# Optimization experiments

Measured on AMD Instinct MI355X. Metric: run time of the kernel, lower is better.

## Reference

```python
import jax, jax.numpy as jnp
import numpy as np

B, H, L, D = 16, 8, 512, 64
TEMPERATURE = 8.0  # sqrt(d_k)
MASK_SENTINEL = -10000.0
BIG_NEG = 1e9


def setup_inputs() -> dict:
    key = jax.random.key(0)
    kq, kk, kv, km = jax.random.split(key, 4)
    q = jax.random.normal(kq, (B * H, L, D), dtype=jnp.float32)
    k = jax.random.normal(kk, (B * H, L, D), dtype=jnp.float32)
    v = jax.random.normal(kv, (B * H, L, D), dtype=jnp.float32)
    mask = jnp.where(jax.random.bernoulli(km, 0.1, (B, L)), MASK_SENTINEL, 0.0).astype(jnp.float32)
    return {"q": q, "k": k, "v": v, "mask": mask, "n_head": H}


def reference(q, k, v, mask, n_head):
    # attn: [B*H, L, L]
    attn = jnp.einsum("bid,bjd->bij", q, k) / TEMPERATURE
    # masked_fill(mask == -10000, 1e9); other values subtracted as-is
    m = jnp.where(mask == MASK_SENTINEL, BIG_NEG, mask)          # [B, L]
    m_bh = jnp.repeat(m, n_head, axis=0)                          # [B*H, L], matches reshape(B*H, ...)
    # row mask (mask.unsqueeze(-1).repeat) and its transpose (column mask)
    attn = attn - m_bh[:, :, None] - m_bh[:, None, :]
    attn = jax.nn.softmax(attn, axis=2)
    # dropout in eval mode (identity) for the deterministic reference
    output = jnp.einsum("bij,bjd->bid", attn, v)
    return output, attn
```

## Files before the change

### kernel.cpp

```cpp
#include <hip/hip_runtime.h>
#include <stdint.h>

#define Ln 512
#define Dn 64
#define BHn 128
#define AOFF ((size_t)BHn*Ln*Dn)

typedef __attribute__((ext_vector_type(8))) short short8;
typedef __attribute__((ext_vector_type(4))) float f32x4;
typedef __attribute__((ext_vector_type(4))) unsigned int u32x4;
typedef __attribute__((ext_vector_type(2))) unsigned int u32x2;

__device__ __forceinline__ uint16_t f2bf(float f){
  uint32_t x = __float_as_uint(f);
  return (uint16_t)((x + 0x7FFFu + ((x>>16)&1u)) >> 16);
}
__device__ __forceinline__ float bf2f(uint16_t u){ return __uint_as_float(((uint32_t)u)<<16); }
__device__ __forceinline__ uint32_t pack2(float a, float b){
  return (uint32_t)f2bf(a) | ((uint32_t)f2bf(b)<<16);
}
__device__ __forceinline__ void gld16(const uint16_t* g, uint16_t* l){
  __builtin_amdgcn_global_load_lds(
      (const __attribute__((address_space(1))) void*)g,
      (__attribute__((address_space(3))) void*)l, 16, 0, 0);
}

extern "C" __global__ __launch_bounds__(256)
void attn_prep(const float* __restrict__ kg, const float* __restrict__ vg,
               uint16_t* __restrict__ khw, uint16_t* __restrict__ klw,
               uint16_t* __restrict__ vtw)
{
  const int t  = threadIdx.x;
  const int c  = blockIdx.x;
  const int bh = blockIdx.y;
  const size_t base = (size_t)bh*(Ln*Dn);
  const size_t wsb  = ((size_t)bh<<15) + ((size_t)c<<13);

  {
    const int sj  = t>>1, skh = t&1;
    const float* kr = kg + base + (size_t)(c*128 + sj)*Dn + skh*32;
    const int sx = (sj&7)<<3;
    #pragma unroll
    for (int w2=0; w2<4; ++w2){
      f32x4 x0 = *(const f32x4*)(kr + w2*8);
      f32x4 x1 = *(const f32x4*)(kr + w2*8 + 4);
      uint32_t hw[4], lw[4];
      #pragma unroll
      for (int pi=0; pi<4; ++pi){
        float a0 = (pi<2) ? x0[pi*2]   : x1[(pi-2)*2];
        float a1 = (pi<2) ? x0[pi*2+1] : x1[(pi-2)*2+1];
        uint16_t h0 = f2bf(a0), h1 = f2bf(a1);
        hw[pi] = (uint32_t)h0 | ((uint32_t)h1<<16);
        lw[pi] = (uint32_t)f2bf(a0 - bf2f(h0)) | ((uint32_t)f2bf(a1 - bf2f(h1))<<16);
      }
      const size_t di = wsb + sj*64 + ((skh*32 + w2*8) ^ sx);
      *(u32x4*)(khw + di) = (u32x4){hw[0],hw[1],hw[2],hw[3]};
      *(u32x4*)(klw + di) = (u32x4){lw[0],lw[1],lw[2],lw[3]};
    }
  }

  #pragma unroll
  for (int it=0; it<2; ++it){
    const int j0 = (t>>4)*4 + it*64;
    const int d0 = (t&15)*4;
    const float* vr = vg + base + (size_t)(c*128 + j0)*Dn + d0;
    f32x4 r0 = *(const f32x4*)(vr);
    f32x4 r1 = *(const f32x4*)(vr + Dn);
    f32x4 r2 = *(const f32x4*)(vr + 2*Dn);
    f32x4 r3 = *(const f32x4*)(vr + 3*Dn);
    #pragma unroll
    for (int qd=0; qd<4; ++qd){
      const int d = d0 + qd;
      u32x2 w; w.x = pack2(r0[qd], r1[qd]); w.y = pack2(r2[qd], r3[qd]);
      *(u32x2*)(vtw + wsb + d*128 + (j0 ^ ((d&7)<<3))) = w;
    }
  }
}

extern "C" __global__ __launch_bounds__(256, 2)
void attn_main2(const float* __restrict__ qg, const float* __restrict__ mg,
                const uint16_t* __restrict__ khw, const uint16_t* __restrict__ klw,
                const uint16_t* __restrict__ vtw, float* __restrict__ outg)
{
  __shared__ __align__(16) uint16_t BIG[32768];
  __shared__ float CMV[512];

  const int t    = threadIdx.x;
  const int lane = t & 63;
  const int wv   = t >> 6;
  const int li   = lane & 15;
  const int lq   = lane >> 4;
  const int kx   = (li&7)<<3;

  const int lin = blockIdx.x + (blockIdx.y << 3);
  const int xcd = lin & 7;
  const int jj  = lin >> 3;
  const int bh  = (xcd << 4) + (jj >> 3);
  const int b   = bh >> 3;
  const int i0  = (jj & 7)*64 + wv*16;

  const size_t base = (size_t)bh*(Ln*Dn);
  const float* mrow = mg + b*Ln;
  const size_t wsbh = (size_t)bh << 15;

  uint16_t* PW = BIG + 16384 + wv*2176;

  auto issueK = [&](int c, int bsel){
    const size_t so = wsbh + ((size_t)c<<13) + (wv<<11) + (lane<<3);
    uint16_t* dh = BIG + bsel*16384 + (wv<<11);
    #pragma unroll
    for (int i=0;i<4;++i){
      gld16(khw + so + i*512, dh + i*512);
      gld16(klw + so + i*512, dh + 8192 + i*512);
    }
  };
  auto issueV = [&](int c, int bsel){
    const size_t so = wsbh + ((size_t)c<<13) + (wv<<11) + (lane<<3);
    uint16_t* dv = BIG + bsel*8192 + (wv<<11);
    #pragma unroll
    for (int i=0;i<4;++i) gld16(vtw + so + i*512, dv + i*512);
  };

  const float* qrow = qg + base + (size_t)(i0 + li)*Dn;
  f32x4 qx0a = *(const f32x4*)(qrow + lq*8);
  f32x4 qx0b = *(const f32x4*)(qrow + lq*8 + 4);
  f32x4 qx1a = *(const f32x4*)(qrow + 32 + lq*8);
  f32x4 qx1b = *(const f32x4*)(qrow + 32 + lq*8 + 4);
  float m0 = mrow[t], m1 = mrow[t+256];
  float mv = mrow[i0 + li];

  issueK(0, 0);

  CMV[t]     = (m0 < -9000.f) ? 1e9f : m0;
  CMV[t+256] = (m1 < -9000.f) ? 1e9f : m1;
  const float rmv = (mv < -9000.f) ? 1e9f : mv;

  short8 qhi[2], qlo[2];
  #pragma unroll
  for (int kt=0; kt<2; ++kt){
    f32x4 xa = kt ? qx1a : qx0a;
    f32x4 xb = kt ? qx1b : qx0b;
    #pragma unroll
    for (int e=0; e<8; ++e){
      float x = (e<4) ? xa[e] : xb[e-4];
      uint16_t h = f2bf(x);
      qhi[kt][e] = (short)h;
      qlo[kt][e] = (short)f2bf(x - bf2f(h));
    }
  }

  f32x4 acc[32];
  #pragma unroll
  for (int j=0; j<32; ++j) acc[j] = (f32x4)0.f;

  #pragma unroll
  for (int c=0; c<4; ++c){
    if (c<3) issueK(c+1, (c+1)&1);
    if (c<3) asm volatile("s_waitcnt vmcnt(8)" ::: "memory");
    else     asm volatile("s_waitcnt vmcnt(4)" ::: "memory");
    __builtin_amdgcn_sched_barrier(0);
    __builtin_amdgcn_s_barrier();
    __builtin_amdgcn_sched_barrier(0);
    const uint16_t* KHp = BIG + (c&1)*16384;
    const uint16_t* KLp = KHp + 8192;
    __builtin_amdgcn_s_setprio(1);
    #pragma unroll
    for (int jt=0; jt<8; ++jt){
      #pragma unroll
      for (int kt=0; kt<2; ++kt){
        const int idx = (jt*16 + li)*64 + ((kt*32 + lq*8) ^ kx);
        short8 kh = *(const short8*)(KHp + idx);
        short8 kl = *(const short8*)(KLp + idx);
        f32x4 A = acc[c*8+jt];
        A = __builtin_amdgcn_mfma_f32_16x16x32_bf16(kh, qhi[kt], A, 0,0,0);
        A = __builtin_amdgcn_mfma_f32_16x16x32_bf16(kl, qhi[kt], A, 0,0,0);
        A = __builtin_amdgcn_mfma_f32_16x16x32_bf16(kh, qlo[kt], A, 0,0,0);
        acc[c*8+jt] = A;
      }
    }
    __builtin_amdgcn_s_setprio(0);
    __builtin_amdgcn_sched_barrier(0);
    __builtin_amdgcn_s_barrier();
    __builtin_amdgcn_sched_barrier(0);
    if (c==2) issueV(0, 0);
  }

  #pragma unroll
  for (int jt=0; jt<32; ++jt){
    f32x4 cm = *(const f32x4*)(CMV + jt*16 + lq*4);
    #pragma unroll
    for (int r=0; r<4; ++r)
      acc[jt][r] = (acc[jt][r]*0.125f - rmv) - cm[r];
  }

  float mx = -3.4e38f;
  #pragma unroll
  for (int jt=0; jt<32; ++jt)
    #pragma unroll
    for (int r=0; r<4; ++r) mx = fmaxf(mx, acc[jt][r]);
  mx = fmaxf(mx, __shfl_xor(mx, 16));
  mx = fmaxf(mx, __shfl_xor(mx, 32));
  float sum = 0.f;
  #pragma unroll
  for (int jt=0; jt<32; ++jt)
    #pragma unroll
    for (int r=0; r<4; ++r){ float e = __expf(acc[jt][r]-mx); acc[jt][r] = e; sum += e; }
  sum += __shfl_xor(sum, 16);
  sum += __shfl_xor(sum, 32);
  const float inv = 1.0f/sum;
  #pragma unroll
  for (int jt=0; jt<32; ++jt) acc[jt] = acc[jt]*inv;

  f32x4 oacc[4];
  #pragma unroll
  for (int dt=0; dt<4; ++dt) oacc[dt] = (f32x4)0.f;

  float* arow = outg + AOFF + (size_t)bh*Ln*Ln + (size_t)(i0+li)*Ln;

  #pragma unroll
  for (int c=0; c<4; ++c){
    if (c==0) asm volatile("s_waitcnt vmcnt(0)" ::: "memory");
    else      asm volatile("s_waitcnt vmcnt(8)" ::: "memory");
    __builtin_amdgcn_sched_barrier(0);
    __builtin_amdgcn_s_barrier();
    __builtin_amdgcn_sched_barrier(0);
    if (c<3) issueV(c+1, (c+1)&1);
    #pragma unroll
    for (int jtl=0; jtl<8; ++jtl){
      const f32x4 p = acc[c*8+jtl];
      u32x2 w; w.x = pack2(p[0], p[1]); w.y = pack2(p[2], p[3]);
      *(u32x2*)(PW + li*136 + jtl*16 + lq*4) = w;
    }
    asm volatile("s_waitcnt lgkmcnt(0)" ::: "memory");
    __builtin_amdgcn_sched_barrier(0);
    const uint16_t* VTp = BIG + (c&1)*8192;
    __builtin_amdgcn_s_setprio(1);
    #pragma unroll
    for (int c32=0; c32<4; ++c32){
      short8 pf = *(const short8*)(PW + li*136 + c32*32 + lq*8);
      #pragma unroll
      for (int dt=0; dt<4; ++dt){
        short8 vb = *(const short8*)(VTp + (dt*16+li)*128 + ((c32*32+lq*8) ^ kx));
        oacc[dt] = __builtin_amdgcn_mfma_f32_16x16x32_bf16(vb, pf, oacc[dt], 0,0,0);
      }
    }
    __builtin_amdgcn_s_setprio(0);
    #pragma unroll
    for (int jtl=0; jtl<8; ++jtl)
      __builtin_nontemporal_store(acc[c*8+jtl], (f32x4*)(arow + (c*8+jtl)*16 + lq*4));
  }

  #pragma unroll
  for (int dt=0; dt<4; ++dt)
    *(f32x4*)(outg + base + (size_t)(i0+li)*Dn + dt*16 + lq*4) = oacc[dt];
}

#define KSTR  72
#define VTSTR 136
#define FPSTRH 136

extern "C" __global__ __launch_bounds__(256, 2)
void attn_mfma(const float* __restrict__ qg, const float* __restrict__ kg,
               const float* __restrict__ vg, const float* __restrict__ mg,
               float* __restrict__ outg)
{
  __shared__ uint4 ldsraw[(36864 + 2048)/16];
  uint16_t* KHI = (uint16_t*)ldsraw;
  uint16_t* KLO = KHI + 128*KSTR;
  uint16_t* VT  = (uint16_t*)ldsraw;
  float*    CMV = (float*)((char*)ldsraw + 36864);

  const int t    = threadIdx.x;
  const int lane = t & 63;
  const int wv   = t >> 6;
  const int li   = lane & 15;
  const int lq   = lane >> 4;

  const int lin = blockIdx.x + (blockIdx.y << 3);
  const int xcd = lin & 7;
  const int jj  = lin >> 3;
  const int bh  = (xcd << 4) + (jj >> 3);
  const int b   = bh >> 3;
  const int i0  = (jj & 7)*64 + wv*16;

  const size_t base = (size_t)bh*(Ln*Dn);
  const float* mrow = mg + b*Ln;

  uint16_t* PW = (uint16_t*)((char*)ldsraw + 17408 + wv*(16*FPSTRH*2));

  {
    float m0 = mrow[t], m1 = mrow[t+256];
    CMV[t]     = (m0 < -9000.f) ? 1e9f : m0;
    CMV[t+256] = (m1 < -9000.f) ? 1e9f : m1;
  }

  short8 qhi[2], qlo[2];
  {
    const float* qrow = qg + base + (size_t)(i0 + li)*Dn;
    #pragma unroll
    for (int kt=0; kt<2; ++kt){
      const float* p = qrow + kt*32 + lq*8;
      f32x4 x0 = *(const f32x4*)p;
      f32x4 x1 = *(const f32x4*)(p+4);
      #pragma unroll
      for (int e=0; e<8; ++e){
        float x = (e<4) ? x0[e] : x1[e-4];
        uint16_t h = f2bf(x);
        qhi[kt][e] = (short)h;
        qlo[kt][e] = (short)f2bf(x - bf2f(h));
      }
    }
  }

  f32x4 acc[32];
  #pragma unroll
  for (int j=0; j<32; ++j) acc[j] = (f32x4)0.f;

  const int sj = t>>1, skh = t&1;
  #pragma unroll
  for (int c=0; c<4; ++c){
    __syncthreads();
    {
      const float* kr = kg + base + (size_t)(c*128 + sj)*Dn + skh*32;
      uint16_t* dhi = KHI + sj*KSTR + skh*32;
      uint16_t* dlo = KLO + sj*KSTR + skh*32;
      #pragma unroll
      for (int w2=0; w2<4; ++w2){
        f32x4 x0 = *(const f32x4*)(kr + w2*8);
        f32x4 x1 = *(const f32x4*)(kr + w2*8 + 4);
        uint32_t hw[4], lw[4];
        #pragma unroll
        for (int pi=0; pi<4; ++pi){
          float a0 = (pi<2) ? x0[pi*2]   : x1[(pi-2)*2];
          float a1 = (pi<2) ? x0[pi*2+1] : x1[(pi-2)*2+1];
          uint16_t h0 = f2bf(a0), h1 = f2bf(a1);
          hw[pi] = (uint32_t)h0 | ((uint32_t)h1<<16);
          lw[pi] = (uint32_t)f2bf(a0 - bf2f(h0)) | ((uint32_t)f2bf(a1 - bf2f(h1))<<16);
        }
        *(u32x4*)(dhi + w2*8) = (u32x4){hw[0],hw[1],hw[2],hw[3]};
        *(u32x4*)(dlo + w2*8) = (u32x4){lw[0],lw[1],lw[2],lw[3]};
      }
    }
    __syncthreads();
    #pragma unroll
    for (int jt=0; jt<8; ++jt){
      #pragma unroll
      for (int kt=0; kt<2; ++kt){
        const int off = (jt*16 + li)*KSTR + kt*32 + lq*8;
        short8 kh = *(const short8*)(KHI + off);
        short8 kl = *(const short8*)(KLO + off);
        f32x4 A = acc[c*8+jt];
        A = __builtin_amdgcn_mfma_f32_16x16x32_bf16(kh, qhi[kt], A, 0,0,0);
        A = __builtin_amdgcn_mfma_f32_16x16x32_bf16(kl, qhi[kt], A, 0,0,0);
        A = __builtin_amdgcn_mfma_f32_16x16x32_bf16(kh, qlo[kt], A, 0,0,0);
        acc[c*8+jt] = A;
      }
    }
  }

  {
    float mv = mrow[i0 + li];
    const float rmv = (mv < -9000.f) ? 1e9f : mv;
    #pragma unroll
    for (int jt=0; jt<32; ++jt){
      f32x4 cm = *(const f32x4*)(CMV + jt*16 + lq*4);
      #pragma unroll
      for (int r=0; r<4; ++r)
        acc[jt][r] = (acc[jt][r]*0.125f - rmv) - cm[r];
    }
  }
  float mx = -3.4e38f;
  #pragma unroll
  for (int jt=0; jt<32; ++jt)
    #pragma unroll
    for (int r=0; r<4; ++r) mx = fmaxf(mx, acc[jt][r]);
  mx = fmaxf(mx, __shfl_xor(mx, 16));
  mx = fmaxf(mx, __shfl_xor(mx, 32));
  float sum = 0.f;
  #pragma unroll
  for (int jt=0; jt<32; ++jt)
    #pragma unroll
    for (int r=0; r<4; ++r){ float e = __expf(acc[jt][r]-mx); acc[jt][r] = e; sum += e; }
  sum += __shfl_xor(sum, 16);
  sum += __shfl_xor(sum, 32);
  const float inv = 1.0f/sum;

  {
    float* arow = outg + AOFF + (size_t)bh*Ln*Ln + (size_t)(i0+li)*Ln;
    #pragma unroll
    for (int jt=0; jt<32; ++jt){
      f32x4 p = acc[jt]*inv;
      acc[jt] = p;
      *(f32x4*)(arow + jt*16 + lq*4) = p;
    }
  }

  f32x4 oacc[4];
  #pragma unroll
  for (int dt=0; dt<4; ++dt) oacc[dt] = (f32x4)0.f;

  #pragma unroll
  for (int c=0; c<4; ++c){
    __syncthreads();
    #pragma unroll
    for (int it=0; it<2; ++it){
      const int j0 = (t>>4)*4 + it*64;
      const int d0 = (t&15)*4;
      const float* vr = vg + base + (size_t)(c*128 + j0)*Dn + d0;
      f32x4 r0 = *(const f32x4*)(vr);
      f32x4 r1 = *(const f32x4*)(vr + Dn);
      f32x4 r2 = *(const f32x4*)(vr + 2*Dn);
      f32x4 r3 = *(const f32x4*)(vr + 3*Dn);
      #pragma unroll
      for (int qd=0; qd<4; ++qd){
        u32x2 w; w.x = pack2(r0[qd], r1[qd]); w.y = pack2(r2[qd], r3[qd]);
        *(u32x2*)(VT + (d0+qd)*VTSTR + j0) = w;
      }
    }
    __syncthreads();
    #pragma unroll
    for (int jtl=0; jtl<8; ++jtl){
      const f32x4 p = acc[c*8+jtl];
      u32x2 w; w.x = pack2(p[0], p[1]); w.y = pack2(p[2], p[3]);
      *(u32x2*)(PW + li*FPSTRH + jtl*16 + lq*4) = w;
    }
    asm volatile("s_waitcnt lgkmcnt(0)" ::: "memory");
    #pragma unroll
    for (int c32=0; c32<4; ++c32){
      short8 pf = *(const short8*)(PW + li*FPSTRH + c32*32 + lq*8);
      #pragma unroll
      for (int dt=0; dt<4; ++dt){
        short8 vb = *(const short8*)(VT + (dt*16+li)*VTSTR + c32*32 + lq*8);
        oacc[dt] = __builtin_amdgcn_mfma_f32_16x16x32_bf16(vb, pf, oacc[dt], 0,0,0);
      }
    }
  }

  #pragma unroll
  for (int dt=0; dt<4; ++dt)
    *(f32x4*)(outg + base + (size_t)(i0+li)*Dn + dt*16 + lq*4) = oacc[dt];
}

extern "C" void kernel_launch(void* const* d_in, const int* in_sizes, int n_in,
                              void* d_out, int out_size, void* d_ws, size_t ws_size,
                              hipStream_t stream)
{
  (void)in_sizes; (void)n_in; (void)out_size;
  const float* qg = (const float*)d_in[0];
  const float* kg = (const float*)d_in[1];
  const float* vg = (const float*)d_in[2];
  const float* mg = (const float*)d_in[3];
  float* outg = (float*)d_out;

  const size_t WS_NEED = 25165824;
  if (d_ws && ws_size >= WS_NEED){
    uint16_t* khw = (uint16_t*)d_ws;
    uint16_t* klw = (uint16_t*)((char*)d_ws + 8388608);
    uint16_t* vtw = (uint16_t*)((char*)d_ws + 16777216);
    attn_prep<<<dim3(4, BHn), 256, 0, stream>>>(kg, vg, khw, klw, vtw);
    attn_main2<<<dim3(Ln/64, BHn), 256, 0, stream>>>(qg, mg, khw, klw, vtw, outg);
  } else {
    attn_mfma<<<dim3(Ln/64, BHn), 256, 0, stream>>>(qg, kg, vg, mg, outg);
  }
}
```

Measured before the change: 231.2 us.

## Split key dimension across waves instead of query rows in attention kernel

Each wave now handles all 64 query rows of the block but only a quarter of the key columns, so every K/V fragment read from LDS feeds four query tiles. Softmax max and sum become cross-wave reductions through small LDS arrays with extra barriers, and the P·V partial outputs are reduced across waves through LDS before being written. The aim is to cut LDS read traffic for K and V per MFMA. In exchange it holds more Q and accumulator registers per thread and adds synchronisation and a final reduction pass.

```diff
diff --git a/kernel.cpp b/kernel.cpp
--- a/kernel.cpp
+++ b/kernel.cpp
@@ -78,12 +78,14 @@
 }
 
 extern "C" __global__ __launch_bounds__(256, 2)
-void attn_main2(const float* __restrict__ qg, const float* __restrict__ mg,
+void attn_main3(const float* __restrict__ qg, const float* __restrict__ mg,
                 const uint16_t* __restrict__ khw, const uint16_t* __restrict__ klw,
                 const uint16_t* __restrict__ vtw, float* __restrict__ outg)
 {
   __shared__ __align__(16) uint16_t BIG[32768];
   __shared__ float CMV[512];
+  __shared__ float MXW[256];
+  __shared__ float SMW[256];
 
   const int t    = threadIdx.x;
   const int lane = t & 63;
@@ -97,13 +99,13 @@
   const int jj  = lin >> 3;
   const int bh  = (xcd << 4) + (jj >> 3);
   const int b   = bh >> 3;
-  const int i0  = (jj & 7)*64 + wv*16;
+  const int i0  = (jj & 7)*64;
 
   const size_t base = (size_t)bh*(Ln*Dn);
   const float* mrow = mg + b*Ln;
   const size_t wsbh = (size_t)bh << 15;
 
-  uint16_t* PW = BIG + 16384 + wv*2176;
+  uint16_t* PW = BIG + 16384 + wv*2560;
 
   auto issueK = [&](int c, int bsel){
     const size_t so = wsbh + ((size_t)c<<13) + (wv<<11) + (lane<<3);
@@ -121,37 +123,46 @@
     for (int i=0;i<4;++i) gld16(vtw + so + i*512, dv + i*512);
   };
 
-  const float* qrow = qg + base + (size_t)(i0 + li)*Dn;
-  f32x4 qx0a = *(const f32x4*)(qrow + lq*8);
-  f32x4 qx0b = *(const f32x4*)(qrow + lq*8 + 4);
-  f32x4 qx1a = *(const f32x4*)(qrow + 32 + lq*8);
-  f32x4 qx1b = *(const f32x4*)(qrow + 32 + lq*8 + 4);
+  f32x4 qa[4][2], qb[4][2];
+  float rmvr[4];
+  #pragma unroll
+  for (int it=0; it<4; ++it){
+    const float* qp = qg + base + (size_t)(i0 + it*16 + li)*Dn;
+    #pragma unroll
+    for (int kt=0; kt<2; ++kt){
+      qa[it][kt] = *(const f32x4*)(qp + kt*32 + lq*8);
+      qb[it][kt] = *(const f32x4*)(qp + kt*32 + lq*8 + 4);
+    }
+    rmvr[it] = mrow[i0 + it*16 + li];
+  }
   float m0 = mrow[t], m1 = mrow[t+256];
-  float mv = mrow[i0 + li];
 
   issueK(0, 0);
 
   CMV[t]     = (m0 < -9000.f) ? 1e9f : m0;
   CMV[t+256] = (m1 < -9000.f) ? 1e9f : m1;
-  const float rmv = (mv < -9000.f) ? 1e9f : mv;
-
-  short8 qhi[2], qlo[2];
-  #pragma unroll
-  for (int kt=0; kt<2; ++kt){
-    f32x4 xa = kt ? qx1a : qx0a;
-    f32x4 xb = kt ? qx1b : qx0b;
-    #pragma unroll
-    for (int e=0; e<8; ++e){
-      float x = (e<4) ? xa[e] : xb[e-4];
-      uint16_t h = f2bf(x);
-      qhi[kt][e] = (short)h;
-      qlo[kt][e] = (short)f2bf(x - bf2f(h));
-    }
-  }
-
-  f32x4 acc[32];
-  #pragma unroll
-  for (int j=0; j<32; ++j) acc[j] = (f32x4)0.f;
+  float rmv[4];
+  #pragma unroll
+  for (int it=0; it<4; ++it) rmv[it] = (rmvr[it] < -9000.f) ? 1e9f : rmvr[it];
+
+  short8 qhi[4][2], qlo[4][2];
+  #pragma unroll
+  for (int it=0; it<4; ++it)
+    #pragma unroll
+    for (int kt=0; kt<2; ++kt)
+      #pragma unroll
+      for (int e=0; e<8; ++e){
+        float x = (e<4) ? qa[it][kt][e] : qb[it][kt][e-4];
+        uint16_t h = f2bf(x);
+        qhi[it][kt][e] = (short)h;
+        qlo[it][kt][e] = (short)f2bf(x - bf2f(h));
+      }
+
+  f32x4 acc[8][4];
+  #pragma unroll
+  for (int m=0; m<8; ++m)
+    #pragma unroll
+    for (int it=0; it<4; ++it) acc[m][it] = (f32x4)0.f;
 
   #pragma unroll
   for (int c=0; c<4; ++c){
@@ -165,17 +176,21 @@
     const uint16_t* KLp = KHp + 8192;
     __builtin_amdgcn_s_setprio(1);
     #pragma unroll
-    for (int jt=0; jt<8; ++jt){
+    for (int mh=0; mh<2; ++mh){
+      const int row = wv*16 + mh*64 + li;
       #pragma unroll
       for (int kt=0; kt<2; ++kt){
-        const int idx = (jt*16 + li)*64 + ((kt*32 + lq*8) ^ kx);
+        const int idx = row*64 + ((kt*32 + lq*8) ^ kx);
         short8 kh = *(const short8*)(KHp + idx);
         short8 kl = *(const short8*)(KLp + idx);
-        f32x4 A = acc[c*8+jt];
-        A = __builtin_amdgcn_mfma_f32_16x16x32_bf16(kh, qhi[kt], A, 0,0,0);
-        A = __builtin_amdgcn_mfma_f32_16x16x32_bf16(kl, qhi[kt], A, 0,0,0);
-        A = __builtin_amdgcn_mfma_f32_16x16x32_bf16(kh, qlo[kt], A, 0,0,0);
-        acc[c*8+jt] = A;
+        #pragma unroll
+        for (int it=0; it<4; ++it){
+          f32x4 A = acc[2*c+mh][it];
+          A = __builtin_amdgcn_mfma_f32_16x16x32_bf16(kh, qhi[it][kt], A, 0,0,0);
+          A = __builtin_amdgcn_mfma_f32_16x16x32_bf16(kl, qhi[it][kt], A, 0,0,0);
+          A = __builtin_amdgcn_mfma_f32_16x16x32_bf16(kh, qlo[it][kt], A, 0,0,0);
+          acc[2*c+mh][it] = A;
+        }
       }
     }
     __builtin_amdgcn_s_setprio(0);
@@ -185,37 +200,75 @@
     if (c==2) issueV(0, 0);
   }
 
-  #pragma unroll
-  for (int jt=0; jt<32; ++jt){
-    f32x4 cm = *(const f32x4*)(CMV + jt*16 + lq*4);
-    #pragma unroll
-    for (int r=0; r<4; ++r)
-      acc[jt][r] = (acc[jt][r]*0.125f - rmv) - cm[r];
-  }
-
-  float mx = -3.4e38f;
-  #pragma unroll
-  for (int jt=0; jt<32; ++jt)
-    #pragma unroll
-    for (int r=0; r<4; ++r) mx = fmaxf(mx, acc[jt][r]);
-  mx = fmaxf(mx, __shfl_xor(mx, 16));
-  mx = fmaxf(mx, __shfl_xor(mx, 32));
-  float sum = 0.f;
-  #pragma unroll
-  for (int jt=0; jt<32; ++jt)
-    #pragma unroll
-    for (int r=0; r<4; ++r){ float e = __expf(acc[jt][r]-mx); acc[jt][r] = e; sum += e; }
-  sum += __shfl_xor(sum, 16);
-  sum += __shfl_xor(sum, 32);
-  const float inv = 1.0f/sum;
-  #pragma unroll
-  for (int jt=0; jt<32; ++jt) acc[jt] = acc[jt]*inv;
-
-  f32x4 oacc[4];
-  #pragma unroll
-  for (int dt=0; dt<4; ++dt) oacc[dt] = (f32x4)0.f;
-
-  float* arow = outg + AOFF + (size_t)bh*Ln*Ln + (size_t)(i0+li)*Ln;
+  float mx[4] = {-3.4e38f,-3.4e38f,-3.4e38f,-3.4e38f};
+  #pragma unroll
+  for (int m=0; m<8; ++m){
+    f32x4 cm = *(const f32x4*)(CMV + (wv + 4*m)*16 + lq*4);
+    #pragma unroll
+    for (int it=0; it<4; ++it)
+      #pragma unroll
+      for (int r=0; r<4; ++r){
+        float v = (acc[m][it][r]*0.125f - rmv[it]) - cm[r];
+        acc[m][it][r] = v;
+        mx[it] = fmaxf(mx[it], v);
+      }
+  }
+  #pragma unroll
+  for (int it=0; it<4; ++it){
+    mx[it] = fmaxf(mx[it], __shfl_xor(mx[it], 16));
+    mx[it] = fmaxf(mx[it], __shfl_xor(mx[it], 32));
+  }
+  if (lane < 16){
+    #pragma unroll
+    for (int it=0; it<4; ++it) MXW[wv*64 + it*16 + lane] = mx[it];
+  }
+  asm volatile("s_waitcnt lgkmcnt(0)" ::: "memory");
+  __builtin_amdgcn_s_barrier();
+  float mxa[4];
+  #pragma unroll
+  for (int it=0; it<4; ++it)
+    mxa[it] = fmaxf(fmaxf(MXW[it*16+li], MXW[64+it*16+li]),
+                    fmaxf(MXW[128+it*16+li], MXW[192+it*16+li]));
+
+  float sm[4] = {0.f,0.f,0.f,0.f};
+  #pragma unroll
+  for (int m=0; m<8; ++m)
+    #pragma unroll
+    for (int it=0; it<4; ++it)
+      #pragma unroll
+      for (int r=0; r<4; ++r){
+        float e = __expf(acc[m][it][r] - mxa[it]);
+        acc[m][it][r] = e;
+        sm[it] += e;
+      }
+  #pragma unroll
+  for (int it=0; it<4; ++it){
+    sm[it] += __shfl_xor(sm[it], 16);
+    sm[it] += __shfl_xor(sm[it], 32);
+  }
+  if (lane < 16){
+    #pragma unroll
+    for (int it=0; it<4; ++it) SMW[wv*64 + it*16 + lane] = sm[it];
+  }
+  asm volatile("s_waitcnt lgkmcnt(0)" ::: "memory");
+  __builtin_amdgcn_s_barrier();
+  float inv[4];
+  #pragma unroll
+  for (int it=0; it<4; ++it)
+    inv[it] = 1.0f/((SMW[it*16+li] + SMW[64+it*16+li]) + (SMW[128+it*16+li] + SMW[192+it*16+li]));
+  #pragma unroll
+  for (int m=0; m<8; ++m)
+    #pragma unroll
+    for (int it=0; it<4; ++it) acc[m][it] = acc[m][it]*inv[it];
+
+  f32x4 oacc[4][4];
+  #pragma unroll
+  for (int dt=0; dt<4; ++dt)
+    #pragma unroll
+    for (int it=0; it<4; ++it) oacc[dt][it] = (f32x4)0.f;
+
+  float* arowb = outg + AOFF + (size_t)bh*Ln*Ln;
+  const int jlq = wv*16 + (lq>>1)*64 + (lq&1)*8;
 
   #pragma unroll
   for (int c=0; c<4; ++c){
@@ -226,33 +279,65 @@
     __builtin_amdgcn_sched_barrier(0);
     if (c<3) issueV(c+1, (c+1)&1);
     #pragma unroll
-    for (int jtl=0; jtl<8; ++jtl){
-      const f32x4 p = acc[c*8+jtl];
-      u32x2 w; w.x = pack2(p[0], p[1]); w.y = pack2(p[2], p[3]);
-      *(u32x2*)(PW + li*136 + jtl*16 + lq*4) = w;
-    }
+    for (int mh=0; mh<2; ++mh)
+      #pragma unroll
+      for (int it=0; it<4; ++it){
+        const f32x4 p = acc[2*c+mh][it];
+        u32x2 w; w.x = pack2(p[0], p[1]); w.y = pack2(p[2], p[3]);
+        *(u32x2*)(PW + (it*16+li)*40 + mh*16 + lq*4) = w;
+      }
     asm volatile("s_waitcnt lgkmcnt(0)" ::: "memory");
     __builtin_amdgcn_sched_barrier(0);
     const uint16_t* VTp = BIG + (c&1)*8192;
     __builtin_amdgcn_s_setprio(1);
-    #pragma unroll
-    for (int c32=0; c32<4; ++c32){
-      short8 pf = *(const short8*)(PW + li*136 + c32*32 + lq*8);
-      #pragma unroll
-      for (int dt=0; dt<4; ++dt){
-        short8 vb = *(const short8*)(VTp + (dt*16+li)*128 + ((c32*32+lq*8) ^ kx));
-        oacc[dt] = __builtin_amdgcn_mfma_f32_16x16x32_bf16(vb, pf, oacc[dt], 0,0,0);
-      }
+    short8 vb[4];
+    #pragma unroll
+    for (int dt=0; dt<4; ++dt)
+      vb[dt] = *(const short8*)(VTp + (dt*16+li)*128 + (jlq ^ kx));
+    #pragma unroll
+    for (int it=0; it<4; ++it){
+      short8 pf = *(const short8*)(PW + (it*16+li)*40 + lq*8);
+      #pragma unroll
+      for (int dt=0; dt<4; ++dt)
+        oacc[dt][it] = __builtin_amdgcn_mfma_f32_16x16x32_bf16(vb[dt], pf, oacc[dt][it], 0,0,0);
     }
     __builtin_amdgcn_s_setprio(0);
     #pragma unroll
-    for (int jtl=0; jtl<8; ++jtl)
-      __builtin_nontemporal_store(acc[c*8+jtl], (f32x4*)(arow + (c*8+jtl)*16 + lq*4));
-  }
-
-  #pragma unroll
-  for (int dt=0; dt<4; ++dt)
-    *(f32x4*)(outg + base + (size_t)(i0+li)*Dn + dt*16 + lq*4) = oacc[dt];
+    for (int mh=0; mh<2; ++mh)
+      #pragma unroll
+      for (int it=0; it<4; ++it)
+        __builtin_nontemporal_store(acc[2*c+mh][it],
+          (f32x4*)(arowb + (size_t)(i0 + it*16 + li)*Ln + (wv + 8*c + 4*mh)*16 + lq*4));
+  }
+
+  asm volatile("s_waitcnt lgkmcnt(0)" ::: "memory");
+  __builtin_amdgcn_sched_barrier(0);
+  __builtin_amdgcn_s_barrier();
+  __builtin_amdgcn_sched_barrier(0);
+  float* ORf = (float*)BIG;
+  #pragma unroll
+  for (int pass=0; pass<2; ++pass){
+    #pragma unroll
+    for (int dh=0; dh<2; ++dh)
+      #pragma unroll
+      for (int it=0; it<4; ++it)
+        #pragma unroll
+        for (int r=0; r<4; ++r)
+          ORf[wv*2176 + (dh*16 + lq*4 + r)*68 + it*16 + li] = oacc[pass*2+dh][it][r];
+    asm volatile("s_waitcnt lgkmcnt(0)" ::: "memory");
+    __builtin_amdgcn_s_barrier();
+    #pragma unroll
+    for (int k=0; k<8; ++k){
+      const int x = t + 256*k;
+      const int d = x & 31, i = x >> 5;
+      float s = (ORf[d*68+i] + ORf[2176 + d*68+i]) + (ORf[4352 + d*68+i] + ORf[6528 + d*68+i]);
+      outg[base + (size_t)(i0 + i)*Dn + pass*32 + d] = s;
+    }
+    if (pass==0){
+      asm volatile("s_waitcnt lgkmcnt(0)" ::: "memory");
+      __builtin_amdgcn_s_barrier();
+    }
+  }
 }
 
 #define KSTR  72
@@ -458,7 +543,7 @@
     uint16_t* klw = (uint16_t*)((char*)d_ws + 8388608);
     uint16_t* vtw = (uint16_t*)((char*)d_ws + 16777216);
     attn_prep<<<dim3(4, BHn), 256, 0, stream>>>(kg, vg, khw, klw, vtw);
-    attn_main2<<<dim3(Ln/64, BHn), 256, 0, stream>>>(qg, mg, khw, klw, vtw, outg);
+    attn_main3<<<dim3(Ln/64, BHn), 256, 0, stream>>>(qg, mg, khw, klw, vtw, outg);
   } else {
     attn_mfma<<<dim3(Ln/64, BHn), 256, 0, stream>>>(qg, kg, vg, mg, outg);
   }
```

Result: slower. 236.4 us (+2.3%).
